# Optimization experiments

Measured on AMD Instinct MI355X. Metric: run time of the kernel, lower is better.

The kernel has to match this reference:

```python
import jax, jax.numpy as jnp
import numpy as np

TEMPERATURE = 0.07
UNIFORMITY_THRESHOLD = 0.1
SEPARATION_MARGIN = 2.0
W_SUPCON = 1.0
W_SEPARATION = 0.5
W_UNIFORMITY = 0.5
NUM_MASKS = 6


def setup_inputs() -> dict:
    key = jax.random.key(0)
    k1, k2, k3 = jax.random.split(key, 3)
    B, H, Wd, D = 16, 33, 33, 512
    emb = jax.random.normal(k1, (B, H, Wd, D), dtype=jnp.float32)
    emb = emb / jnp.linalg.norm(emb, axis=-1, keepdims=True)  # module expects normalized embeddings
    masks = jax.random.uniform(k2, (B, NUM_MASKS, H, Wd), dtype=jnp.float32)
    is_forged = jax.random.uniform(k3, (B,), dtype=jnp.float32)
    return {"embeddings": emb, "masks": masks, "is_forged": is_forged}


def _labels(masks):
    # masks: (M, H, W). Channel i writes label i+1 where mask>0.5 (if channel has any mass);
    # later channels overwrite earlier -> equivalent to max over active hits.
    active = masks.sum(axis=(1, 2)) > 0  # (M,)
    hit = (masks > 0.5) & active[:, None, None]
    ids = jnp.arange(1, masks.shape[0] + 1)[:, None, None]
    return jnp.max(jnp.where(hit, ids, 0), axis=0).reshape(-1)  # (H*W,)


def _per_image(emb, masks, forged):
    H, W, D = emb.shape
    feat = emb.reshape(-1, D)  # (N, D)
    N = feat.shape[0]
    labels = _labels(masks)  # (N,) in 0..M
    L = masks.shape[0] + 1  # possible labels 0..6
    onehot = (labels[:, None] == jnp.arange(L)[None, :]).astype(feat.dtype)  # (N, L)
    cnt = onehot.sum(axis=0)  # (L,)
    sums = onehot.T @ feat  # (L, D) per-label sums
    mean_l = sums / jnp.maximum(cnt, 1.0)[:, None]  # safe per-label centroids

    # ---- SupCon (PixelSupConLoss) ----
    logits = (feat @ feat.T) / TEMPERATURE  # (N, N)
    logits = logits - jax.lax.stop_gradient(logits.max(axis=1, keepdims=True))
    same = (labels[:, None] == labels[None, :]).astype(feat.dtype)
    logits_mask = 1.0 - jnp.eye(N, dtype=feat.dtype)
    pos = same * logits_mask
    exp_l = jnp.exp(logits) * logits_mask
    log_prob = logits - jnp.log(exp_l.sum(axis=1, keepdims=True) + 1e-6)
    pos_sum = pos.sum(axis=1)
    mean_lp = (pos * log_prob).sum(axis=1) / jnp.where(pos_sum == 0, 1.0, pos_sum)
    anchor_valid = (pos_sum > 0).astype(feat.dtype)
    n_anchor = anchor_valid.sum()
    supcon = (-mean_lp * anchor_valid).sum() / jnp.maximum(n_anchor, 1.0)
    supcon_valid = n_anchor > 0

    # ---- Inter-instance separation ----
    present = cnt > 0
    cn = (mean_l ** 2).sum(axis=1)  # (L,)
    sq = cn[:, None] + cn[None, :] - 2.0 * (mean_l @ mean_l.T)  # squared centroid dists
    tri = jnp.triu(jnp.ones((L, L), dtype=bool), k=1)
    pair_valid = tri & present[:, None] & present[None, :]
    d = jnp.sqrt(jnp.where(pair_valid, jnp.maximum(sq, 0.0), 1.0))
    terms = jnp.where(pair_valid, jax.nn.relu(SEPARATION_MARGIN - d), 0.0)
    n_pairs = pair_valid.sum().astype(feat.dtype)
    sep = terms.sum() / jnp.maximum(n_pairs, 1.0)
    sep_valid = present.sum() >= 2

    # ---- Uniformity ----
    rn2 = (feat ** 2).sum(axis=1)  # (N,)
    q_l = onehot.T @ rn2  # (L,) per-label sum of squared norms
    var_l = q_l / jnp.maximum(cnt, 1.0) - (mean_l ** 2).sum(axis=1)  # E||e||^2 - ||mean||^2
    lbl_valid = (cnt >= 2) & (var_l > UNIFORMITY_THRESHOLD)
    inst_loss = jnp.where(lbl_valid, var_l - UNIFORMITY_THRESHOLD, 0.0).sum()
    n_lbl = lbl_valid.sum().astype(feat.dtype)
    uni_forged = inst_loss / jnp.maximum(n_lbl, 1.0)
    uni_forged_valid = n_lbl > 0
    mean_all = feat.mean(axis=0)
    var_all = ((feat - mean_all) ** 2).sum(axis=1).mean()
    uni_unf = jnp.where(var_all > UNIFORMITY_THRESHOLD, var_all - UNIFORMITY_THRESHOLD, 0.0)
    uni_unf_valid = var_all > UNIFORMITY_THRESHOLD

    is_f = forged >= 0.5
    uni = jnp.where(is_f, uni_forged, uni_unf)
    uni_valid = jnp.where(is_f, uni_forged_valid, uni_unf_valid)
    return supcon, supcon_valid, sep, sep_valid, uni, uni_valid


def _agg(vals, valids):
    v = valids.astype(vals.dtype)
    n = v.sum()
    return jnp.where(n > 0, (vals * v).sum() / jnp.maximum(n, 1.0), 0.0)


def reference(embeddings, masks, is_forged):
    sc, scv, sp, spv, un, unv = jax.vmap(_per_image)(embeddings, masks, is_forged)
    supcon = _agg(sc, scv)
    separation = _agg(sp, spv)
    uniformity = _agg(un, unv)
    return W_SUPCON * supcon + W_SEPARATION * separation + W_UNIFORMITY * uniformity
```

## Files before the change

kernel.cpp:

```cpp
#include <hip/hip_runtime.h>
#include <math.h>

#define NPIX 1089
#define DIM 512
#define NIMG 16
#define NLBL 8
#define NMASK 6
#define INVT 14.2857142857142857f

#define NGRP 72
#define NT9 9



typedef short v8s __attribute__((ext_vector_type(8)));
typedef float v4f __attribute__((ext_vector_type(4)));

__device__ __forceinline__ float wave_reduce(float x) {
#pragma unroll
  for (int o = 32; o > 0; o >>= 1) x += __shfl_xor(x, o, 64);
  return x;
}
__device__ __forceinline__ unsigned bfbits(float x) {
  unsigned u = __float_as_uint(x);
  return (u + 0x7FFFu + ((u >> 16) & 1u)) >> 16;
}
__device__ __forceinline__ unsigned pk(float lo, float hi) {
  return bfbits(lo) | (bfbits(hi) << 16);
}

__global__ void k_labels(const float* __restrict__ masks, int* __restrict__ labels,
                         float* __restrict__ cnt) {
  int b = blockIdx.x, tid = threadIdx.x;
  int lane = tid & 63, w = tid >> 6;
  __shared__ float msum[NMASK];
  __shared__ float red[4][NLBL];
  if (tid < NMASK) msum[tid] = 0.f;
  __syncthreads();
  float acc[NMASK] = {0.f, 0.f, 0.f, 0.f, 0.f, 0.f};
  for (int p = tid; p < NPIX; p += 256) {
#pragma unroll
    for (int c = 0; c < NMASK; c++) acc[c] += masks[((size_t)b * NMASK + c) * NPIX + p];
  }
#pragma unroll
  for (int c = 0; c < NMASK; c++) {
    float v = wave_reduce(acc[c]);
    if (lane == 0) atomicAdd(&msum[c], v);
  }
  __syncthreads();
  float c8[NLBL] = {0.f, 0.f, 0.f, 0.f, 0.f, 0.f, 0.f, 0.f};
  for (int p = tid; p < NPIX; p += 256) {
    int lab = 0;
#pragma unroll
    for (int c = 0; c < NMASK; c++) {
      float mv = masks[((size_t)b * NMASK + c) * NPIX + p];
      if (mv > 0.5f && msum[c] > 0.f) lab = c + 1;
    }
    labels[b * NPIX + p] = lab;
#pragma unroll
    for (int l = 0; l < NLBL; l++) c8[l] += (lab == l) ? 1.f : 0.f;
  }
#pragma unroll
  for (int l = 0; l < NLBL; l++) c8[l] = wave_reduce(c8[l]);
  if (lane == 0) {
#pragma unroll
    for (int l = 0; l < NLBL; l++) red[w][l] = c8[l];
  }
  __syncthreads();
  if (tid < NLBL)
    cnt[b * NLBL + tid] = red[0][tid] + red[1][tid] + red[2][tid] + red[3][tid];
}

__global__ __launch_bounds__(512) void k_packsum(const float* __restrict__ emb,
                                                 const int* __restrict__ labels,
                                                 uint2* __restrict__ bfemb2,
                                                 float* __restrict__ sums) {
  int b = blockIdx.y;
  int g9 = blockIdx.x >> 1, dh = blockIdx.x & 1;
  int tid = threadIdx.x, dd = tid & 63, w4 = tid >> 6;
  __shared__ int slab[128];
  __shared__ float4 red[8 * 8 * 64];
  if (tid < 128) {
    int r = g9 * 128 + tid;
    slab[tid] = (r < NPIX) ? labels[b * NPIX + r] : 7;
  }
  __syncthreads();
  float4 fa0 = {0,0,0,0}, fa1 = {0,0,0,0}, fa2 = {0,0,0,0}, fa3 = {0,0,0,0};
  float4 fa4 = {0,0,0,0}, fa5 = {0,0,0,0}, fa6 = {0,0,0,0}, fa7 = {0,0,0,0};
  int kc = dh * 8 + (dd >> 3), q = (dd >> 1) & 3, half = dd & 1;
#pragma unroll
  for (int k = 0; k < 16; k++) {
    int r = g9 * 128 + w4 + k * 8;
    bool v = r < NPIX;
    int rc = v ? r : (NPIX - 1);
    float4 x = ((const float4*)(emb + (size_t)(b * NPIX + rc) * DIM))[dh * 64 + dd];
    if (!v) x = make_float4(0.f, 0.f, 0.f, 0.f);
    uint2 o = make_uint2(pk(x.x, x.y), pk(x.z, x.w));
    bfemb2[((((size_t)(b * NGRP + (r >> 4)) * 16 + kc) * 64) + q * 16 + (r & 15)) * 2 + half] = o;
    int lab = __builtin_amdgcn_readfirstlane(slab[r - g9 * 128]);
    switch (lab) {
      case 0: fa0.x += x.x; fa0.y += x.y; fa0.z += x.z; fa0.w += x.w; break;
      case 1: fa1.x += x.x; fa1.y += x.y; fa1.z += x.z; fa1.w += x.w; break;
      case 2: fa2.x += x.x; fa2.y += x.y; fa2.z += x.z; fa2.w += x.w; break;
      case 3: fa3.x += x.x; fa3.y += x.y; fa3.z += x.z; fa3.w += x.w; break;
      case 4: fa4.x += x.x; fa4.y += x.y; fa4.z += x.z; fa4.w += x.w; break;
      case 5: fa5.x += x.x; fa5.y += x.y; fa5.z += x.z; fa5.w += x.w; break;
      case 6: fa6.x += x.x; fa6.y += x.y; fa6.z += x.z; fa6.w += x.w; break;
      default: fa7.x += x.x; fa7.y += x.y; fa7.z += x.z; fa7.w += x.w; break;
    }
  }
  red[(0 * 8 + w4) * 64 + dd] = fa0; red[(1 * 8 + w4) * 64 + dd] = fa1;
  red[(2 * 8 + w4) * 64 + dd] = fa2; red[(3 * 8 + w4) * 64 + dd] = fa3;
  red[(4 * 8 + w4) * 64 + dd] = fa4; red[(5 * 8 + w4) * 64 + dd] = fa5;
  red[(6 * 8 + w4) * 64 + dd] = fa6; red[(7 * 8 + w4) * 64 + dd] = fa7;
  __syncthreads();
  int l = tid >> 6, d2 = tid & 63;
  float4 s = {0,0,0,0};
#pragma unroll
  for (int ww = 0; ww < 8; ww++) {
    float4 t = red[(l * 8 + ww) * 64 + d2];
    s.x += t.x; s.y += t.y; s.z += t.z; s.w += t.w;
  }
  float* dst = &sums[((size_t)b * NLBL + l) * DIM + dh * 256 + d2 * 4];
  atomicAdd(dst + 0, s.x); atomicAdd(dst + 1, s.y);
  atomicAdd(dst + 2, s.z); atomicAdd(dst + 3, s.w);
}

__global__ __launch_bounds__(256) void k_epass3(const uint4* __restrict__ bfemb4,
                                                float* __restrict__ E) {
  int n = blockIdx.x;
  int img = ((n & 7) << 1) | ((n >> 3) & 1);
  int t = n >> 4;
  int it = 0, rem = t;
  while (rem >= NT9 - it) { rem -= NT9 - it; it++; }
  int jt = it + rem;
  int i0 = it * 128, j0 = jt * 128;
  bool diag = (it == jt);
  int tid = threadIdx.x, lane = tid & 63, w = tid >> 6;
  int wm = w >> 1, wn = w & 1;
  int quad = lane >> 4, l15 = lane & 15;

  size_t uA[4], uB[4];
#pragma unroll
  for (int f = 0; f < 4; f++) {
    uA[f] = ((size_t)(img * NGRP + it * 8 + wm * 4 + f) * 16) * 64 + lane;
    uB[f] = ((size_t)(img * NGRP + jt * 8 + wn * 4 + f) * 16) * 64 + lane;
  }

  v4f acc[4][4];
#pragma unroll
  for (int mf = 0; mf < 4; mf++)
#pragma unroll
    for (int nf = 0; nf < 4; nf++) acc[mf][nf] = (v4f){0.f, 0.f, 0.f, 0.f};

  v8s a0[4], b0[4], a1[4], b1[4];
#define LOADG(kc, AR, BR)                                               \
  {                                                                     \
    _Pragma("unroll") for (int f = 0; f < 4; f++)                       \
        AR[f] = *(const v8s*)(bfemb4 + uA[f] + (kc) * 64);              \
    _Pragma("unroll") for (int f = 0; f < 4; f++)                       \
        BR[f] = *(const v8s*)(bfemb4 + uB[f] + (kc) * 64);              \
  }
#define MFMAG(AR, BR)                                                   \
  {                                                                     \
    _Pragma("unroll") for (int mf = 0; mf < 4; mf++)                    \
        _Pragma("unroll") for (int nf = 0; nf < 4; nf++)                \
            acc[mf][nf] = __builtin_amdgcn_mfma_f32_16x16x32_bf16(      \
                AR[mf], BR[nf], acc[mf][nf], 0, 0, 0);                  \
  }

  LOADG(0, a0, b0);
#pragma unroll
  for (int kc = 0; kc < 16; kc += 2) {
    if (kc + 1 < 16) LOADG(kc + 1, a1, b1);
    MFMAG(a0, b0);
    if (kc + 2 < 16) LOADG(kc + 2, a0, b0);
    MFMAG(a1, b1);
  }
#undef LOADG
#undef MFMAG

  float scol[4] = {0.f, 0.f, 0.f, 0.f};
#pragma unroll
  for (int mf = 0; mf < 4; mf++) {
#pragma unroll
    for (int rr = 0; rr < 4; rr++) {
      int i = i0 + wm * 64 + mf * 16 + quad * 4 + rr;
      float srow = 0.f;
#pragma unroll
      for (int nf = 0; nf < 4; nf++) {
        int j = j0 + wn * 64 + nf * 16 + l15;
        float e = __expf((acc[mf][nf][rr] - 1.f) * INVT);
        bool ok = (j < NPIX) && (!diag || (i != j && i < NPIX));
        e = ok ? e : 0.f;
        srow += e;
        scol[nf] += e;
      }
      srow += __shfl_xor(srow, 1); srow += __shfl_xor(srow, 2);
      srow += __shfl_xor(srow, 4); srow += __shfl_xor(srow, 8);
      if (l15 == 0 && i < NPIX) atomicAdd(&E[img * NPIX + i], srow);
    }
  }
  if (!diag) {
#pragma unroll
    for (int nf = 0; nf < 4; nf++) {
      float s = scol[nf];
      s += __shfl_xor(s, 16); s += __shfl_xor(s, 32);
      int j = j0 + wn * 64 + nf * 16 + l15;
      if (quad == 0 && j < NPIX) atomicAdd(&E[img * NPIX + j], s);
    }
  }
}

__global__ void k_img(const float* __restrict__ sums, const int* __restrict__ labels,
                      const float* __restrict__ cnt, const float* __restrict__ E,
                      const float* __restrict__ is_forged, float* __restrict__ per_img) {
  int b = blockIdx.x, tid = threadIdx.x;
  int wave = tid >> 6, lane = tid & 63;
  __shared__ float sCnt[NLBL], sR[NLBL][NLBL];
  __shared__ float sLog, sNA;
  if (tid < NLBL) sCnt[tid] = cnt[b * NLBL + tid];
  if (tid == 0) { sLog = 0.f; sNA = 0.f; }
  __syncthreads();
  float ll = 0.f, na = 0.f;
  for (int p = tid; p < NPIX; p += 256) {
    int lab = labels[b * NPIX + p];
    if (sCnt[lab] >= 1.5f) { ll += logf(E[b * NPIX + p] + 1e-6f); na += 1.f; }
  }
  ll = wave_reduce(ll); na = wave_reduce(na);
  if (lane == 0) { atomicAdd(&sLog, ll); atomicAdd(&sNA, na); }
  for (int t = wave; t < 36; t += 4) {
    int a = 0, tt = t;
    while (tt >= NLBL - a) { tt -= NLBL - a; a++; }
    int bb = a + tt;
    const float* sa = sums + ((size_t)b * NLBL + a) * DIM;
    const float* sb = sums + ((size_t)b * NLBL + bb) * DIM;
    float d0 = 0.f;
    for (int k = lane; k < DIM; k += 64) d0 += sa[k] * sb[k];
    d0 = wave_reduce(d0);
    if (lane == 0) sR[a][bb] = d0;
  }
  __syncthreads();
  if (tid == 0) {
    float spos = 0.f;
    for (int l = 0; l < NLBL; l++) {
      float c = sCnt[l];
      if (c >= 1.5f) spos += (sR[l][l] - c) * INVT / (c - 1.f) - c * INVT;
    }
    float nA = sNA;
    float sc = nA > 0.f ? (sLog - spos) / nA : 0.f;
    float scv = nA > 0.f ? 1.f : 0.f;
    float inv[NLBL]; int present[NLBL]; int nPres = 0;
    for (int l = 0; l < NLBL; l++) {
      present[l] = sCnt[l] > 0.f;
      nPres += present[l];
      inv[l] = 1.f / fmaxf(sCnt[l], 1.f);
    }
    float sepsum = 0.f; int npairs = 0;
    for (int a = 0; a < NLBL; a++)
      for (int c = a + 1; c < NLBL; c++)
        if (present[a] && present[c]) {
          float sq_ = sR[a][a] * inv[a] * inv[a] + sR[c][c] * inv[c] * inv[c]
                    - 2.f * sR[a][c] * inv[a] * inv[c];
          float dd = sqrtf(fmaxf(sq_, 0.f));
          sepsum += fmaxf(2.f - dd, 0.f);
          npairs++;
        }
    float sep = npairs > 0 ? sepsum / (float)npairs : 0.f;
    float sepv = nPres >= 2 ? 1.f : 0.f;
    float inst = 0.f; int nlbl = 0;
    for (int l = 0; l < NLBL; l++) {
      float var = 1.f - sR[l][l] * inv[l] * inv[l];
      if (sCnt[l] >= 2.f && var > 0.1f) { inst += var - 0.1f; nlbl++; }
    }
    float unif = nlbl > 0 ? inst / (float)nlbl : 0.f;
    float unifv = nlbl > 0 ? 1.f : 0.f;
    float tot2 = 0.f;
    for (int a = 0; a < NLBL; a++) {
      tot2 += sR[a][a];
      for (int c = a + 1; c < NLBL; c++) tot2 += 2.f * sR[a][c];
    }
    float Nf = (float)NPIX;
    float var_all = 1.f - tot2 / (Nf * Nf);
    float uniu = var_all > 0.1f ? var_all - 0.1f : 0.f;
    float uniuv = var_all > 0.1f ? 1.f : 0.f;
    bool isf = is_forged[b] >= 0.5f;
    per_img[b * 6 + 0] = sc;
    per_img[b * 6 + 1] = scv;
    per_img[b * 6 + 2] = sep;
    per_img[b * 6 + 3] = sepv;
    per_img[b * 6 + 4] = isf ? unif : uniu;
    per_img[b * 6 + 5] = isf ? unifv : uniuv;
  }
}

__global__ void k_final(const float* __restrict__ per_img, float* __restrict__ out) {
  if (threadIdx.x == 0) {
    float accv[3] = {0.f, 0.f, 0.f}, accn[3] = {0.f, 0.f, 0.f};
    for (int b = 0; b < NIMG; b++)
      for (int m = 0; m < 3; m++) {
        float v = per_img[b * 6 + m * 2], val = per_img[b * 6 + m * 2 + 1];
        accv[m] += v * val; accn[m] += val;
      }
    float sc = accn[0] > 0.f ? accv[0] / accn[0] : 0.f;
    float sep = accn[1] > 0.f ? accv[1] / accn[1] : 0.f;
    float uni = accn[2] > 0.f ? accv[2] / accn[2] : 0.f;
    out[0] = 1.0f * sc + 0.5f * sep + 0.5f * uni;
  }
}

extern "C" void kernel_launch(void* const* d_in, const int* in_sizes, int n_in,
                              void* d_out, int out_size, void* d_ws, size_t ws_size,
                              hipStream_t stream) {
  const float* emb = (const float*)d_in[0];
  const float* masks = (const float*)d_in[1];
  const float* isf = (const float*)d_in[2];
  float* out = (float*)d_out;
  char* ws = (char*)d_ws;
  size_t off = 0;
  uint4* bfemb4 = (uint4*)(ws + off);
  off += (size_t)NIMG * NGRP * 16 * 64 * 16;
  float* E = (float*)(ws + off);     off += sizeof(float) * NIMG * NPIX;
  float* sums = (float*)(ws + off);  off += sizeof(float) * NIMG * NLBL * DIM;
  int* labels = (int*)(ws + off);    off += sizeof(int) * NIMG * NPIX;
  float* cnt = (float*)(ws + off);   off += sizeof(float) * NIMG * NLBL;
  float* per_img = (float*)(ws + off); off += sizeof(float) * NIMG * 6;

  hipMemsetAsync(E, 0, sizeof(float) * (NIMG * NPIX + NIMG * NLBL * DIM), stream);
  k_labels<<<NIMG, 256, 0, stream>>>(masks, labels, cnt);
  k_packsum<<<dim3(18, NIMG), 512, 0, stream>>>(emb, labels, (uint2*)bfemb4, sums);
  k_epass3<<<45 * NIMG, 256, 0, stream>>>(bfemb4, E);
  k_img<<<NIMG, 256, 0, stream>>>(sums, labels, cnt, E, isf, per_img);
  k_final<<<1, 64, 0, stream>>>(per_img, out);
}
```

Measured before the change: 152.1 us.

## Replace global atomics with per-tile partial buffers and drop memset

```diff
diff --git a/kernel.cpp b/kernel.cpp
--- a/kernel.cpp
+++ b/kernel.cpp
@@ -9,6 +9,7 @@
 #define INVT 14.2857142857142857f
 
 #define NGRP 72
+#define NROWPAD 1152
 #define NT9 9
 
 
@@ -74,7 +75,7 @@
 __global__ __launch_bounds__(512) void k_packsum(const float* __restrict__ emb,
                                                  const int* __restrict__ labels,
                                                  uint2* __restrict__ bfemb2,
-                                                 float* __restrict__ sums) {
+                                                 float* __restrict__ sums9) {
   int b = blockIdx.y;
   int g9 = blockIdx.x >> 1, dh = blockIdx.x & 1;
   int tid = threadIdx.x, dd = tid & 63, w4 = tid >> 6;
@@ -121,13 +122,11 @@
     float4 t = red[(l * 8 + ww) * 64 + d2];
     s.x += t.x; s.y += t.y; s.z += t.z; s.w += t.w;
   }
-  float* dst = &sums[((size_t)b * NLBL + l) * DIM + dh * 256 + d2 * 4];
-  atomicAdd(dst + 0, s.x); atomicAdd(dst + 1, s.y);
-  atomicAdd(dst + 2, s.z); atomicAdd(dst + 3, s.w);
+  *(float4*)&sums9[(((size_t)(b * NT9 + g9) * NLBL + l) * DIM) + dh * 256 + d2 * 4] = s;
 }
 
 __global__ __launch_bounds__(256) void k_epass3(const uint4* __restrict__ bfemb4,
-                                                float* __restrict__ E) {
+                                                float* __restrict__ E18) {
   int n = blockIdx.x;
   int img = ((n & 7) << 1) | ((n >> 3) & 1);
   int t = n >> 4;
@@ -180,6 +179,8 @@
 #undef LOADG
 #undef MFMAG
 
+  float* Erow = E18 + ((size_t)img * 18 + jt * 2 + wn) * NROWPAD;
+  float* Ecol = E18 + ((size_t)img * 18 + it * 2 + wm) * NROWPAD;
   float scol[4] = {0.f, 0.f, 0.f, 0.f};
 #pragma unroll
   for (int mf = 0; mf < 4; mf++) {
@@ -198,7 +199,7 @@
       }
       srow += __shfl_xor(srow, 1); srow += __shfl_xor(srow, 2);
       srow += __shfl_xor(srow, 4); srow += __shfl_xor(srow, 8);
-      if (l15 == 0 && i < NPIX) atomicAdd(&E[img * NPIX + i], srow);
+      if (l15 == 0) Erow[i] = srow;
     }
   }
   if (!diag) {
@@ -207,25 +208,38 @@
       float s = scol[nf];
       s += __shfl_xor(s, 16); s += __shfl_xor(s, 32);
       int j = j0 + wn * 64 + nf * 16 + l15;
-      if (quad == 0 && j < NPIX) atomicAdd(&E[img * NPIX + j], s);
-    }
-  }
-}
-
-__global__ void k_img(const float* __restrict__ sums, const int* __restrict__ labels,
-                      const float* __restrict__ cnt, const float* __restrict__ E,
+      if (quad == 0) Ecol[j] = s;
+    }
+  }
+}
+
+__global__ void k_img(const float* __restrict__ sums9, const int* __restrict__ labels,
+                      const float* __restrict__ cnt, const float* __restrict__ E18,
                       const float* __restrict__ is_forged, float* __restrict__ per_img) {
   int b = blockIdx.x, tid = threadIdx.x;
   int wave = tid >> 6, lane = tid & 63;
+  __shared__ float ssum[NLBL * DIM];
   __shared__ float sCnt[NLBL], sR[NLBL][NLBL];
   __shared__ float sLog, sNA;
   if (tid < NLBL) sCnt[tid] = cnt[b * NLBL + tid];
   if (tid == 0) { sLog = 0.f; sNA = 0.f; }
+  for (int o = tid; o < NLBL * DIM; o += 256) {
+    float s = 0.f;
+#pragma unroll
+    for (int g = 0; g < NT9; g++) s += sums9[((size_t)(b * NT9 + g) * NLBL * DIM) + o];
+    ssum[o] = s;
+  }
   __syncthreads();
   float ll = 0.f, na = 0.f;
   for (int p = tid; p < NPIX; p += 256) {
     int lab = labels[b * NPIX + p];
-    if (sCnt[lab] >= 1.5f) { ll += logf(E[b * NPIX + p] + 1e-6f); na += 1.f; }
+    if (sCnt[lab] >= 1.5f) {
+      float e = 0.f;
+#pragma unroll
+      for (int s = 0; s < 18; s++) e += E18[((size_t)b * 18 + s) * NROWPAD + p];
+      ll += logf(e + 1e-6f);
+      na += 1.f;
+    }
   }
   ll = wave_reduce(ll); na = wave_reduce(na);
   if (lane == 0) { atomicAdd(&sLog, ll); atomicAdd(&sNA, na); }
@@ -233,10 +247,8 @@
     int a = 0, tt = t;
     while (tt >= NLBL - a) { tt -= NLBL - a; a++; }
     int bb = a + tt;
-    const float* sa = sums + ((size_t)b * NLBL + a) * DIM;
-    const float* sb = sums + ((size_t)b * NLBL + bb) * DIM;
     float d0 = 0.f;
-    for (int k = lane; k < DIM; k += 64) d0 += sa[k] * sb[k];
+    for (int k = lane; k < DIM; k += 64) d0 += ssum[a * DIM + k] * ssum[bb * DIM + k];
     d0 = wave_reduce(d0);
     if (lane == 0) sR[a][bb] = d0;
   }
@@ -320,16 +332,15 @@
   size_t off = 0;
   uint4* bfemb4 = (uint4*)(ws + off);
   off += (size_t)NIMG * NGRP * 16 * 64 * 16;
-  float* E = (float*)(ws + off);     off += sizeof(float) * NIMG * NPIX;
-  float* sums = (float*)(ws + off);  off += sizeof(float) * NIMG * NLBL * DIM;
-  int* labels = (int*)(ws + off);    off += sizeof(int) * NIMG * NPIX;
-  float* cnt = (float*)(ws + off);   off += sizeof(float) * NIMG * NLBL;
+  float* E18 = (float*)(ws + off);    off += sizeof(float) * NIMG * 18 * NROWPAD;
+  float* sums9 = (float*)(ws + off);  off += sizeof(float) * NIMG * NT9 * NLBL * DIM;
+  int* labels = (int*)(ws + off);     off += sizeof(int) * NIMG * NPIX;
+  float* cnt = (float*)(ws + off);    off += sizeof(float) * NIMG * NLBL;
   float* per_img = (float*)(ws + off); off += sizeof(float) * NIMG * 6;
 
-  hipMemsetAsync(E, 0, sizeof(float) * (NIMG * NPIX + NIMG * NLBL * DIM), stream);
   k_labels<<<NIMG, 256, 0, stream>>>(masks, labels, cnt);
-  k_packsum<<<dim3(18, NIMG), 512, 0, stream>>>(emb, labels, (uint2*)bfemb4, sums);
-  k_epass3<<<45 * NIMG, 256, 0, stream>>>(bfemb4, E);
-  k_img<<<NIMG, 256, 0, stream>>>(sums, labels, cnt, E, isf, per_img);
+  k_packsum<<<dim3(18, NIMG), 512, 0, stream>>>(emb, labels, (uint2*)bfemb4, sums9);
+  k_epass3<<<45 * NIMG, 256, 0, stream>>>(bfemb4, E18);
+  k_img<<<NIMG, 256, 0, stream>>>(sums9, labels, cnt, E18, isf, per_img);
   k_final<<<1, 64, 0, stream>>>(per_img, out);
 }
```

After: 140.2 us. -7.9%, faster.
